# Performance work log

Measured on AMD Instinct MI355X. Metric: run time of the kernel, lower is better.

Reference implementation:

```python
import jax, jax.numpy as jnp
import numpy as np

N, C, H, W = 16, 64, 128, 128
SHIFT = 1  # frozen value of torch module's random.randint(-2, 2) drawn at __init__


def setup_inputs() -> dict:
    key = jax.random.key(0)
    k1, k2, k3 = jax.random.split(key, 3)
    x = jax.random.normal(k1, (N, C, H, W), dtype=jnp.float32)
    # p_3: Conv2d(c, c, (1,5), padding=(0,2), bias=False) -> weight (C_out, C_in, 1, 5)
    w3 = jax.random.normal(k2, (C, C, 1, 5), dtype=jnp.float32) * (1.0 / np.sqrt(5.0 * C))
    # p_7: Conv2d(9c, c, 1, groups=c, bias=False) -> per output channel, 9 input channels: (C, 9)
    w7 = jax.random.normal(k3, (C, 9), dtype=jnp.float32) * (1.0 / 3.0)
    return {"x": x, "w3": w3, "w7": w7}


def reference(x, w3, w7):
    n, c, h, w = x.shape
    # t_1: F.unfold(x, (1,3), dilation=(1,2), padding=(0,2)) -> width offsets -2, 0, +2 (zero padded)
    xp = jnp.pad(x, ((0, 0), (0, 0), (0, 0), (2, 2)))
    t1 = jnp.stack([xp[..., 0:w], xp[..., 2:w + 2], xp[..., 4:w + 4]], axis=2)  # (n,c,3,h,w)
    # t_3: 1x5 conv, padding (0,2)
    t3 = jax.lax.conv_general_dilated(
        x, w3, window_strides=(1, 1), padding=[(0, 0), (2, 2)],
        dimension_numbers=("NCHW", "OIHW", "NCHW"))  # (n,c,h,w)
    # t_4: F.unfold(t1 as (n,3c,h,w), (3,1), padding=(1,0)) -> height offsets -1, 0, +1
    t1p = jnp.pad(t1, ((0, 0), (0, 0), (0, 0), (1, 1), (0, 0)))
    t4 = jnp.stack([t1p[..., 0:h, :], t1p[..., 1:h + 1, :], t1p[..., 2:h + 2, :]],
                   axis=3)  # (n, c, 3[w_off], 3[h_off], h, w)
    # t_5: roll along the W axis (dim 5)
    t5 = jnp.roll(t4, SHIFT, axis=5)
    # t_6: maximum of lhs (n,c,1,3,h,w) and rhs (n,c,3,3,h,w); lhs offset dim aligns with rhs dim 3
    t6 = jnp.maximum(t1[:, :, None, :, :, :], t5)  # (n,c,3,3,h,w)
    # t_7: grouped 1x1 conv, groups=c, 9 input channels per group -> 1 output channel
    t6f = t6.reshape(n, c, 9, h, w)
    t7 = jnp.einsum("nckhw,ck->nchw", t6f, w7)
    return t7 * t3
```

## Files before the change

kernel.cpp:

```cpp
#include <hip/hip_runtime.h>

#define NN 16
#define CC 64
#define HH 128
#define WW 128

#define LDS_STRIDE 72
#define T3_STRIDE 132

typedef __attribute__((ext_vector_type(8))) short short8;
typedef __attribute__((ext_vector_type(4))) float floatx4;

__device__ __forceinline__ short f2bf(float f) {
    union { float f; unsigned u; } v; v.f = f;
    unsigned r = v.u + 0x7fffu + ((v.u >> 16) & 1u);
    return (short)(r >> 16);
}

__global__ __launch_bounds__(256) void prep_w(const float* __restrict__ w3,
                                              short* __restrict__ Abf) {
    int idx = blockIdx.x * 256 + threadIdx.x;
    if (idx < CC * CC * 5) {
        int tap = idx % 5;
        int ci  = (idx / 5) % CC;
        int co  = idx / (5 * CC);
        Abf[co * 320 + tap * 64 + ci] = f2bf(w3[idx]);
    }
}

__global__ __launch_bounds__(256) void fused(const float* __restrict__ x,
                                             const short* __restrict__ Abf,
                                             const float* __restrict__ w7,
                                             float* __restrict__ out) {
    __shared__ __align__(16) char smem[CC * T3_STRIDE * 4];
    short* xsT = (short*)smem;
    float* t3s = (float*)smem;

    const int nh  = blockIdx.x;
    const int n   = nh >> 7;
    const int h   = nh & (HH - 1);
    const int tid = threadIdx.x;

    const float* xbase = x + (((size_t)n * CC) * HH + h) * WW;
    #pragma unroll
    for (int i = 0; i < 8; ++i) {
        int idx = tid + i * 256;
        int ci  = idx >> 5;
        int wq  = idx & 31;
        float4 v = *(const float4*)(xbase + (size_t)ci * (HH * WW) + wq * 4);
        int wp = wq * 4 + 2;
        xsT[(wp + 0) * LDS_STRIDE + ci] = f2bf(v.x);
        xsT[(wp + 1) * LDS_STRIDE + ci] = f2bf(v.y);
        xsT[(wp + 2) * LDS_STRIDE + ci] = f2bf(v.z);
        xsT[(wp + 3) * LDS_STRIDE + ci] = f2bf(v.w);
    }
    {
        int wpi = tid >> 6;
        int wpz = (wpi < 2) ? wpi : 128 + wpi;
        int ci  = tid & 63;
        xsT[wpz * LDS_STRIDE + ci] = 0;
    }
    __syncthreads();

    const int W    = tid >> 6;
    const int lane = tid & 63;
    const int lm   = lane & 15;
    const int g    = lane >> 4;

    floatx4 acc[8];
    #pragma unroll
    for (int nt = 0; nt < 8; ++nt) acc[nt] = (floatx4){0.f, 0.f, 0.f, 0.f};

    const short* arow = Abf + (W * 16 + lm) * 320;

    for (int ks = 0; ks < 10; ++ks) {
        const int kbase = ks * 32 + g * 8;
        const int tap   = kbase >> 6;
        const int cib   = kbase & 63;

        short8 a = *(const short8*)(arow + kbase);
        #pragma unroll
        for (int nt = 0; nt < 8; ++nt) {
            int wp = nt * 16 + lm + tap;
            short8 b = *(const short8*)&xsT[wp * LDS_STRIDE + cib];
            acc[nt] = __builtin_amdgcn_mfma_f32_16x16x32_bf16(a, b, acc[nt], 0, 0, 0);
        }
    }
    __syncthreads();

    #pragma unroll
    for (int nt = 0; nt < 8; ++nt) {
        #pragma unroll
        for (int r = 0; r < 4; ++r) {
            int co = W * 16 + g * 4 + r;
            t3s[co * T3_STRIDE + nt * 16 + lm] = acc[nt][r];
        }
    }
    __syncthreads();

    float* orow = out + (((size_t)n * CC) * HH + h) * WW;
    #pragma unroll
    for (int it = 0; it < 8; ++it) {
        const int item = it * 256 + tid;
        const int flat = item * 4;
        const int w0   = flat & (WW - 1);
        const int c    = flat >> 7;
        const float* xb = x + ((size_t)(n * CC + c) * HH) * WW;

        float win[3][12];
        #pragma unroll
        for (int r = 0; r < 3; ++r) {
            int hh = h + r - 1;
            bool hok = (unsigned)hh < HH;
            #pragma unroll
            for (int q = 0; q < 3; ++q) {
                int cb = w0 - 4 + q * 4;
                float4 v = make_float4(0.f, 0.f, 0.f, 0.f);
                if (hok && (unsigned)cb < WW)
                    v = *(const float4*)(xb + hh * WW + cb);
                win[r][q * 4 + 0] = v.x; win[r][q * 4 + 1] = v.y;
                win[r][q * 4 + 2] = v.z; win[r][q * 4 + 3] = v.w;
            }
        }
        float wrap0[3] = {0.f, 0.f, 0.f}, wrap1[3] = {0.f, 0.f, 0.f};
        if (w0 == 0) {
            #pragma unroll
            for (int r = 0; r < 3; ++r) {
                int hh = h + r - 1;
                if ((unsigned)hh < HH) {
                    wrap0[r] = xb[hh * WW + 125];
                    wrap1[r] = xb[hh * WW + 127];
                }
            }
        }
        float wc[9];
        #pragma unroll
        for (int t = 0; t < 9; ++t) wc[t] = w7[c * 9 + t];

        float4 t3v = *(const float4*)&t3s[c * T3_STRIDE + w0];
        float res[4];
        #pragma unroll
        for (int e = 0; e < 4; ++e) {
            float a = 0.f;
            #pragma unroll
            for (int j = 0; j < 3; ++j) {
                #pragma unroll
                for (int i = 0; i < 3; ++i) {
                    float lhs = win[1][e + 2 * i + 2];
                    float rhs;
                    if (e == 0 && w0 == 0)
                        rhs = (j == 0) ? wrap0[i] : ((j == 1) ? wrap1[i] : 0.f);
                    else
                        rhs = win[i][e + 2 * j + 1];
                    a = fmaf(wc[j * 3 + i], fmaxf(lhs, rhs), a);
                }
            }
            res[e] = a;
        }
        float4 o;
        o.x = res[0] * t3v.x; o.y = res[1] * t3v.y;
        o.z = res[2] * t3v.z; o.w = res[3] * t3v.w;
        *(float4*)(orow + (size_t)c * (HH * WW) + w0) = o;
    }
}

extern "C" void kernel_launch(void* const* d_in, const int* in_sizes, int n_in,
                              void* d_out, int out_size, void* d_ws, size_t ws_size,
                              hipStream_t stream) {
    const float* x  = (const float*)d_in[0];
    const float* w3 = (const float*)d_in[1];
    const float* w7 = (const float*)d_in[2];
    float* out = (float*)d_out;

    short* Abf = (short*)d_ws;

    prep_w<<<(CC * CC * 5 + 255) / 256, 256, 0, stream>>>(w3, Abf);
    fused<<<NN * HH, 256, 0, stream>>>(x, Abf, w7, out);
}
```

Measured before the change: 154.2 us.

## Store t3 in LDS as bf16 and pack channel pairs into 32-bit stores

```diff
diff --git a/kernel.cpp b/kernel.cpp
--- a/kernel.cpp
+++ b/kernel.cpp
@@ -6,7 +6,7 @@
 #define WW 128
 
 #define LDS_STRIDE 72
-#define T3_STRIDE 132
+#define T3B_STRIDE 132
 
 typedef __attribute__((ext_vector_type(8))) short short8;
 typedef __attribute__((ext_vector_type(4))) float floatx4;
@@ -15,6 +15,16 @@
     union { float f; unsigned u; } v; v.f = f;
     unsigned r = v.u + 0x7fffu + ((v.u >> 16) & 1u);
     return (short)(r >> 16);
+}
+__device__ __forceinline__ unsigned pack2bf(float lo, float hi) {
+    union { float f; unsigned u; } a, b; a.f = lo; b.f = hi;
+    unsigned ra = a.u + 0x7fffu + ((a.u >> 16) & 1u);
+    unsigned rb = b.u + 0x7fffu + ((b.u >> 16) & 1u);
+    return (ra >> 16) | (rb & 0xffff0000u);
+}
+__device__ __forceinline__ float bf2f(unsigned short u) {
+    union { unsigned u; float f; } v; v.u = ((unsigned)u) << 16;
+    return v.f;
 }
 
 __global__ __launch_bounds__(256) void prep_w(const float* __restrict__ w3,
@@ -28,13 +38,14 @@
     }
 }
 
-__global__ __launch_bounds__(256) void fused(const float* __restrict__ x,
-                                             const short* __restrict__ Abf,
-                                             const float* __restrict__ w7,
-                                             float* __restrict__ out) {
-    __shared__ __align__(16) char smem[CC * T3_STRIDE * 4];
-    short* xsT = (short*)smem;
-    float* t3s = (float*)smem;
+__global__ __launch_bounds__(256, 8) void fused(const float* __restrict__ x,
+                                                const short* __restrict__ Abf,
+                                                const float* __restrict__ w7,
+                                                float* __restrict__ out) {
+    __shared__ __align__(16) char smem[132 * LDS_STRIDE * 2];
+    short*    xsT = (short*)smem;
+    unsigned* xsW = (unsigned*)smem;
+    short*    t3b = (short*)smem;
 
     const int nh  = blockIdx.x;
     const int n   = nh >> 7;
@@ -42,23 +53,27 @@
     const int tid = threadIdx.x;
 
     const float* xbase = x + (((size_t)n * CC) * HH + h) * WW;
-    #pragma unroll
-    for (int i = 0; i < 8; ++i) {
-        int idx = tid + i * 256;
-        int ci  = idx >> 5;
-        int wq  = idx & 31;
-        float4 v = *(const float4*)(xbase + (size_t)ci * (HH * WW) + wq * 4);
-        int wp = wq * 4 + 2;
-        xsT[(wp + 0) * LDS_STRIDE + ci] = f2bf(v.x);
-        xsT[(wp + 1) * LDS_STRIDE + ci] = f2bf(v.y);
-        xsT[(wp + 2) * LDS_STRIDE + ci] = f2bf(v.z);
-        xsT[(wp + 3) * LDS_STRIDE + ci] = f2bf(v.w);
-    }
     {
-        int wpi = tid >> 6;
-        int wpz = (wpi < 2) ? wpi : 128 + wpi;
-        int ci  = tid & 63;
-        xsT[wpz * LDS_STRIDE + ci] = 0;
+        const int cp  = tid & 31;
+        const int wqg = tid >> 5;
+        const float* r0 = xbase + (size_t)(2 * cp) * (HH * WW);
+        const float* r1 = r0 + HH * WW;
+        #pragma unroll
+        for (int q = 0; q < 4; ++q) {
+            int wq = wqg * 4 + q;
+            float4 a = *(const float4*)(r0 + wq * 4);
+            float4 b = *(const float4*)(r1 + wq * 4);
+            int wp = wq * 4 + 2;
+            xsW[(wp + 0) * 36 + cp] = pack2bf(a.x, b.x);
+            xsW[(wp + 1) * 36 + cp] = pack2bf(a.y, b.y);
+            xsW[(wp + 2) * 36 + cp] = pack2bf(a.z, b.z);
+            xsW[(wp + 3) * 36 + cp] = pack2bf(a.w, b.w);
+        }
+        if (tid < 128) {
+            int wpi = tid >> 5;
+            int wpz = (wpi < 2) ? wpi : 128 + wpi;
+            xsW[wpz * 36 + (tid & 31)] = 0u;
+        }
     }
     __syncthreads();
 
@@ -93,7 +108,7 @@
         #pragma unroll
         for (int r = 0; r < 4; ++r) {
             int co = W * 16 + g * 4 + r;
-            t3s[co * T3_STRIDE + nt * 16 + lm] = acc[nt][r];
+            t3b[co * T3B_STRIDE + nt * 16 + lm] = f2bf(acc[nt][r]);
         }
     }
     __syncthreads();
@@ -137,7 +152,9 @@
         #pragma unroll
         for (int t = 0; t < 9; ++t) wc[t] = w7[c * 9 + t];
 
-        float4 t3v = *(const float4*)&t3s[c * T3_STRIDE + w0];
+        ushort4 tv = *(const ushort4*)&t3b[c * T3B_STRIDE + w0];
+        float t3v[4] = {bf2f(tv.x), bf2f(tv.y), bf2f(tv.z), bf2f(tv.w)};
+
         float res[4];
         #pragma unroll
         for (int e = 0; e < 4; ++e) {
@@ -158,8 +175,8 @@
             res[e] = a;
         }
         float4 o;
-        o.x = res[0] * t3v.x; o.y = res[1] * t3v.y;
-        o.z = res[2] * t3v.z; o.w = res[3] * t3v.w;
+        o.x = res[0] * t3v[0]; o.y = res[1] * t3v[1];
+        o.z = res[2] * t3v[2]; o.w = res[3] * t3v[3];
         *(float4*)(orow + (size_t)c * (HH * WW) + w0) = o;
     }
 }
```

New measurement: 158.6 us. 2.8% more time.
